# Optimization experiments

Hardware: AMD Instinct MI355X
Metric: run time of the kernel (lower is better)

The kernel has to match this reference:

```python
import jax, jax.numpy as jnp
import numpy as np

B, D, H, W = 16, 512, 32, 32   # batch, input_dim, spatial
CD, K = 256, 8192              # codebook dim, num codes
COMMIT = 1.0


def setup_inputs() -> dict:
    key = jax.random.key(0)
    k0, k1, k2, k3 = jax.random.split(key, 4)
    x = jax.random.normal(k0, (B, D, H, W), dtype=jnp.float32)
    # project_in: Linear(D -> CD); project_out: Linear(CD -> D)
    W_in = jax.random.normal(k1, (CD, D), dtype=jnp.float32) * (1.0 / np.sqrt(D))
    b_in = jnp.zeros((CD,), dtype=jnp.float32)
    W_out = jax.random.normal(k2, (D, CD), dtype=jnp.float32) * (1.0 / np.sqrt(CD))
    b_out = jnp.zeros((D,), dtype=jnp.float32)
    codebook = jax.random.normal(k3, (K, CD), dtype=jnp.float32) * 0.05
    return {"x": x, "W_in": W_in, "b_in": b_in, "W_out": W_out,
            "b_out": b_out, "codebook": codebook}


def reference(x, W_in, b_in, W_out, b_out, codebook):
    b, d, h, w = x.shape
    # b d h w -> b (h w) d
    xt = x.reshape(b, d, h * w).transpose(0, 2, 1)
    z = xt @ W_in.T + b_in                              # [b, n, CD]
    # squared euclidean distances to all codes: ||z||^2 - 2 z.e + ||e||^2
    d2 = ((z * z).sum(-1, keepdims=True)
          - 2.0 * jnp.einsum('bnc,kc->bnk', z, codebook)
          + (codebook * codebook).sum(-1))              # [b, n, K]
    indices = jnp.argmin(d2, axis=-1)                   # [b, n] int
    q = codebook[indices]                               # [b, n, CD]
    # training branch: commitment loss + straight-through estimator
    commitment_loss = COMMIT * jnp.mean((jax.lax.stop_gradient(q) - z) ** 2)
    q_ste = z + jax.lax.stop_gradient(q - z)
    out = q_ste @ W_out.T + b_out                       # [b, n, d]
    out = out.transpose(0, 2, 1).reshape(b, d, h, w)    # b (h w) d -> b d h w
    return out, indices, commitment_loss
```

## Files before the change

### kernel.cpp

```cpp
#include <hip/hip_runtime.h>
#include <cfloat>
#include <cstdint>

#define B_      16
#define DIN     512
#define HW      1024
#define CDIM    256
#define KCODES  8192
#define NTOK    (B_ * HW)
#define OUT_ELEMS (B_ * DIN * HW)
#define NSTRIP  8
#define NPART2  64
#define CPS     (KCODES / NSTRIP)
#define MAXR    4096
#define RCHUNK  32
#define RBLOCKS 2048
#define LOSS_SCALE (1.0f / ((float)NTOK * (float)CDIM))
#define WSCALE      16.0f
#define INV_WS      0.0625f
#define INV_WS2     0.00390625f
#define NEG2_INV_WS (-0.125f)
#define BAND_SLACK  2e-3f

typedef __attribute__((ext_vector_type(8))) _Float16 f16x8;
typedef __attribute__((ext_vector_type(4))) float f32x4;

static __device__ __forceinline__ short f2h(float f) {
  _Float16 h = (_Float16)f;
  return __builtin_bit_cast(short, h);
}
static __device__ __forceinline__ float h2f(short h) {
  return (float)__builtin_bit_cast(_Float16, h);
}

#define GLL16(gsrc, ldst)                                                      \
  __builtin_amdgcn_global_load_lds(                                           \
      (const __attribute__((address_space(1))) unsigned int*)(gsrc),          \
      (__attribute__((address_space(3))) unsigned int*)(ldst), 16, 0, 0)

#define PREP_CB_BLKS 2048
#define PREP_W_BLKS  128
#define PREP_X_BLKS  2048
__global__ __launch_bounds__(256) void k_prep(
    const float* __restrict__ cb, const float* __restrict__ Win,
    const float* __restrict__ Wout, const float* __restrict__ x,
    short* __restrict__ cb_hi, short* __restrict__ cb_lo, float* __restrict__ ee,
    short* __restrict__ wi_hi, short* __restrict__ wi_lo,
    short* __restrict__ wo_hi,
    short* __restrict__ xT_hi, short* __restrict__ xT_lo,
    float* __restrict__ loss, int* __restrict__ rcount, int* __restrict__ scal) {
  __shared__ float T[64][65];
  const int blk = blockIdx.x;
  const int tid = threadIdx.x;
  if (blk == 0 && tid < 2) {
    if (tid == 0) *loss = 0.0f; else *rcount = 0;
  }
  if (blk < PREP_CB_BLKS) {
    const int wid = (blk * 256 + tid) >> 6;
    const int lane = tid & 63;
    const float4 v = *(const float4*)(cb + (size_t)wid * CDIM + lane * 4);
    float s = v.x * v.x + v.y * v.y + v.z * v.z + v.w * v.w;
    const float sx = v.x * WSCALE, sy = v.y * WSCALE,
                sz = v.z * WSCALE, sw = v.w * WSCALE;
    short4 h, l;
    h.x = f2h(sx); l.x = f2h(sx - h2f(h.x));
    h.y = f2h(sy); l.y = f2h(sy - h2f(h.y));
    h.z = f2h(sz); l.z = f2h(sz - h2f(h.z));
    h.w = f2h(sw); l.w = f2h(sw - h2f(h.w));
    *(short4*)(cb_hi + (size_t)wid * CDIM + lane * 4) = h;
    *(short4*)(cb_lo + (size_t)wid * CDIM + lane * 4) = l;
    const float rx = v.x - h2f(h.x) * INV_WS;
    const float ry = v.y - h2f(h.y) * INV_WS;
    const float rz = v.z - h2f(h.z) * INV_WS;
    const float rw = v.w - h2f(h.w) * INV_WS;
    float rr = rx * rx + ry * ry + rz * rz + rw * rw;
#pragma unroll
    for (int off = 32; off > 0; off >>= 1) {
      s += __shfl_down(s, off, 64);
      rr += __shfl_down(rr, off, 64);
    }
    const int wv = tid >> 6;
    if (lane == 0) { ee[wid] = s; T[0][wv] = s; T[1][wv] = rr; }
    __syncthreads();
    if (tid == 0) {
      const float em = fmaxf(fmaxf(T[0][0], T[0][1]), fmaxf(T[0][2], T[0][3]));
      const float rm = fmaxf(fmaxf(T[1][0], T[1][1]), fmaxf(T[1][2], T[1][3]));
      atomicMax(scal + 0, __float_as_int(em));
      atomicMax(scal + 1, __float_as_int(rm));
    }
  } else if (blk < PREP_CB_BLKS + PREP_W_BLKS) {
    const int i = ((blk - PREP_CB_BLKS) * 256 + tid) * 4;
    {
      const float4 v = *(const float4*)(Win + i);
      const float sx = v.x * WSCALE, sy = v.y * WSCALE,
                  sz = v.z * WSCALE, sw = v.w * WSCALE;
      short4 h, l;
      h.x = f2h(sx); l.x = f2h(sx - h2f(h.x));
      h.y = f2h(sy); l.y = f2h(sy - h2f(h.y));
      h.z = f2h(sz); l.z = f2h(sz - h2f(h.z));
      h.w = f2h(sw); l.w = f2h(sw - h2f(h.w));
      *(short4*)(wi_hi + i) = h; *(short4*)(wi_lo + i) = l;
    }
    {
      const float4 v = *(const float4*)(Wout + i);
      short4 h;
      h.x = f2h(v.x * WSCALE);
      h.y = f2h(v.y * WSCALE);
      h.z = f2h(v.z * WSCALE);
      h.w = f2h(v.w * WSCALE);
      *(short4*)(wo_hi + i) = h;
    }
  } else {
    const int id = blk - PREP_CB_BLKS - PREP_W_BLKS;
    const int xb = id & 255, yb = id >> 8;
    const int b = xb >> 4;
    const int hw0 = (xb & 15) * 64;
    const int din0 = yb * 64;
    {
      const int r = tid >> 2;
      const int c = tid & 3;
      const float* src = x + ((size_t)b * DIN + din0 + r) * HW + hw0 + c * 16;
#pragma unroll
      for (int j = 0; j < 4; ++j) {
        const float4 v = *(const float4*)(src + j * 4);
        T[r][c * 16 + j * 4 + 0] = v.x;
        T[r][c * 16 + j * 4 + 1] = v.y;
        T[r][c * 16 + j * 4 + 2] = v.z;
        T[r][c * 16 + j * 4 + 3] = v.w;
      }
    }
    __syncthreads();
    {
      const int tt = tid & 63;
      const int c2 = tid >> 6;
      short h[16], l[16];
#pragma unroll
      for (int j = 0; j < 16; ++j) {
        const float f = T[c2 * 16 + j][tt];
        h[j] = f2h(f); l[j] = f2h(f - h2f(h[j]));
      }
      const size_t base = ((size_t)b * HW + hw0 + tt) * DIN + din0 + c2 * 16;
      *(f16x8*)(xT_hi + base)     = *(f16x8*)&h[0];
      *(f16x8*)(xT_hi + base + 8) = *(f16x8*)&h[8];
      *(f16x8*)(xT_lo + base)     = *(f16x8*)&l[0];
      *(f16x8*)(xT_lo + base + 8) = *(f16x8*)&l[8];
    }
  }
}

__global__ __launch_bounds__(256, 2) void k_proj_in_mfma(
    const short* __restrict__ xT_hi, const short* __restrict__ xT_lo,
    const short* __restrict__ wi_hi, const short* __restrict__ wi_lo,
    const float* __restrict__ bin,
    short* __restrict__ z_hi, short* __restrict__ z_lo) {
  __shared__ short lds_s[4 * 128 * 32];
  char* ldsc = (char*)lds_s;
  const int tid = threadIdx.x;
  const int w = tid >> 6, lane = tid & 63;
  const int quad = lane >> 4, l16 = lane & 15;
  const int wm = w >> 1, wn = w & 1;
  const int tok0 = blockIdx.x * 128;
  const int cd0 = blockIdx.y * 128;

  const int uA = (w << 6) + lane, uB = uA + 256;
  const int tA = uA >> 2, pA = uA & 3, qA = pA ^ ((tA >> 1) & 3);
  const int tB = uB >> 2, pB = uB & 3, qB = pB ^ ((tB >> 1) & 3);
  const int offA = tA * DIN + qA * 8;
  const int offB = tB * DIN + qB * 8;
  const short* gAh0 = xT_hi + (size_t)tok0 * DIN + offA;
  const short* gAh1 = xT_hi + (size_t)tok0 * DIN + offB;
  const short* gAl0 = xT_lo + (size_t)tok0 * DIN + offA;
  const short* gAl1 = xT_lo + (size_t)tok0 * DIN + offB;
  const short* gBh0 = wi_hi + (size_t)cd0 * DIN + offA;
  const short* gBh1 = wi_hi + (size_t)cd0 * DIN + offB;
  const short* gBl0 = wi_lo + (size_t)cd0 * DIN + offA;
  const short* gBl1 = wi_lo + (size_t)cd0 * DIN + offB;

  int aoffs[4], boffs[4];
#pragma unroll
  for (int mi = 0; mi < 4; ++mi) {
    const int t = wm * 64 + mi * 16 + l16;
    aoffs[mi] = t * 64 + (quad ^ ((t >> 1) & 3)) * 16;
  }
#pragma unroll
  for (int ni = 0; ni < 4; ++ni) {
    const int t = wn * 64 + ni * 16 + l16;
    boffs[ni] = 16384 + t * 64 + (quad ^ ((t >> 1) & 3)) * 16;
  }

  f32x4 acc[4][4];
#pragma unroll
  for (int mi = 0; mi < 4; ++mi)
#pragma unroll
    for (int ni = 0; ni < 4; ++ni) acc[mi][ni] = (f32x4){0.f, 0.f, 0.f, 0.f};

  for (int kb = 0; kb < DIN; kb += 32) {
    __syncthreads();
    GLL16(gAh0 + kb, ldsc + ((0 * 4 + w) << 10));
    GLL16(gAh1 + kb, ldsc + ((1 * 4 + w) << 10));
    GLL16(gAl0 + kb, ldsc + ((2 * 4 + w) << 10));
    GLL16(gAl1 + kb, ldsc + ((3 * 4 + w) << 10));
    GLL16(gBh0 + kb, ldsc + ((4 * 4 + w) << 10));
    GLL16(gBh1 + kb, ldsc + ((5 * 4 + w) << 10));
    GLL16(gBl0 + kb, ldsc + ((6 * 4 + w) << 10));
    GLL16(gBl1 + kb, ldsc + ((7 * 4 + w) << 10));
    __syncthreads();
    f16x8 ah[4], al[4], bh[4], bl[4];
#pragma unroll
    for (int mi = 0; mi < 4; ++mi) {
      ah[mi] = *(const f16x8*)(ldsc + aoffs[mi]);
      al[mi] = *(const f16x8*)(ldsc + 8192 + aoffs[mi]);
    }
#pragma unroll
    for (int ni = 0; ni < 4; ++ni) {
      bh[ni] = *(const f16x8*)(ldsc + boffs[ni]);
      bl[ni] = *(const f16x8*)(ldsc + 8192 + boffs[ni]);
    }
#pragma unroll
    for (int mi = 0; mi < 4; ++mi)
#pragma unroll
      for (int ni = 0; ni < 4; ++ni) {
        f32x4 c = acc[mi][ni];
        c = __builtin_amdgcn_mfma_f32_16x16x32_f16(ah[mi], bh[ni], c, 0, 0, 0);
        c = __builtin_amdgcn_mfma_f32_16x16x32_f16(ah[mi], bl[ni], c, 0, 0, 0);
        c = __builtin_amdgcn_mfma_f32_16x16x32_f16(al[mi], bh[ni], c, 0, 0, 0);
        acc[mi][ni] = c;
      }
  }
  float bv[4];
#pragma unroll
  for (int ni = 0; ni < 4; ++ni) bv[ni] = bin[cd0 + wn * 64 + ni * 16 + l16];
#pragma unroll
  for (int mi = 0; mi < 4; ++mi)
#pragma unroll
    for (int r = 0; r < 4; ++r) {
      const int t = tok0 + wm * 64 + mi * 16 + quad * 4 + r;
#pragma unroll
      for (int ni = 0; ni < 4; ++ni) {
        const int cd = cd0 + wn * 64 + ni * 16 + l16;
        const float o = acc[mi][ni][r] * INV_WS + bv[ni];
        const short h = f2h(o);
        z_hi[(size_t)t * CDIM + cd] = h;
        z_lo[(size_t)t * CDIM + cd] = f2h(o - h2f(h));
      }
    }
}

__global__ __launch_bounds__(256, 2) void k_argmin_mfma(
    const short* __restrict__ z_hi,
    const short* __restrict__ cb_hi,
    const float* __restrict__ ee,
    float* __restrict__ pm1v, int* __restrict__ pm1i, float* __restrict__ pm2v) {
  __shared__ short lds_s[2 * 128 * 32];
  char* ldsc = (char*)lds_s;
  const int tid = threadIdx.x;
  const int w = tid >> 6, lane = tid & 63;
  const int quad = lane >> 4, l16 = lane & 15;
  const int wm = w >> 1, wn = w & 1;
  const int tok0 = blockIdx.x * 128;
  const int cbase = blockIdx.y * CPS;

  const int uA = (w << 6) + lane, uB = uA + 256;
  const int tA = uA >> 2, pA = uA & 3, qA = pA ^ ((tA >> 1) & 3);
  const int tB = uB >> 2, pB = uB & 3, qB = pB ^ ((tB >> 1) & 3);
  const int offA = tA * CDIM + qA * 8;
  const int offB = tB * CDIM + qB * 8;
  const short* gAh0 = z_hi + (size_t)tok0 * CDIM + offA;
  const short* gAh1 = z_hi + (size_t)tok0 * CDIM + offB;

  int aoffs[4], boffs[4];
#pragma unroll
  for (int mi = 0; mi < 4; ++mi) {
    const int t = wm * 64 + mi * 16 + l16;
    aoffs[mi] = t * 64 + (quad ^ ((t >> 1) & 3)) * 16;
  }
#pragma unroll
  for (int ni = 0; ni < 4; ++ni) {
    const int t = wn * 64 + ni * 16 + l16;
    boffs[ni] = 8192 + t * 64 + (quad ^ ((t >> 1) & 3)) * 16;
  }

  float mv[16], sv[16]; int mi_[16];
#pragma unroll
  for (int j = 0; j < 16; ++j) {
    mv[j] = FLT_MAX; sv[j] = FLT_MAX; mi_[j] = 0x7fffffff;
  }

  for (int ct = 0; ct < CPS / 128; ++ct) {
    const int ctile = cbase + ct * 128;
    const short* gBh0 = cb_hi + (size_t)ctile * CDIM + offA;
    const short* gBh1 = cb_hi + (size_t)ctile * CDIM + offB;
    f32x4 acc[4][4];
#pragma unroll
    for (int mi = 0; mi < 4; ++mi)
#pragma unroll
      for (int ni = 0; ni < 4; ++ni) acc[mi][ni] = (f32x4){0.f, 0.f, 0.f, 0.f};

    for (int kb = 0; kb < CDIM; kb += 32) {
      __syncthreads();
      GLL16(gAh0 + kb, ldsc + ((0 * 4 + w) << 10));
      GLL16(gAh1 + kb, ldsc + ((1 * 4 + w) << 10));
      GLL16(gBh0 + kb, ldsc + ((2 * 4 + w) << 10));
      GLL16(gBh1 + kb, ldsc + ((3 * 4 + w) << 10));
      __syncthreads();
      f16x8 ah[4], bh[4];
#pragma unroll
      for (int mi = 0; mi < 4; ++mi)
        ah[mi] = *(const f16x8*)(ldsc + aoffs[mi]);
#pragma unroll
      for (int ni = 0; ni < 4; ++ni)
        bh[ni] = *(const f16x8*)(ldsc + boffs[ni]);
#pragma unroll
      for (int mi = 0; mi < 4; ++mi)
#pragma unroll
        for (int ni = 0; ni < 4; ++ni)
          acc[mi][ni] = __builtin_amdgcn_mfma_f32_16x16x32_f16(
              ah[mi], bh[ni], acc[mi][ni], 0, 0, 0);
    }
    float eev[4];
#pragma unroll
    for (int ni = 0; ni < 4; ++ni) eev[ni] = ee[ctile + wn * 64 + ni * 16 + l16];
    const int cb2 = ctile + wn * 64 + l16;
#pragma unroll
    for (int mi = 0; mi < 4; ++mi)
#pragma unroll
      for (int r = 0; r < 4; ++r) {
        const int j = mi * 4 + r;
#pragma unroll
        for (int ni = 0; ni < 4; ++ni) {
          const float s = fmaf(NEG2_INV_WS, acc[mi][ni][r], eev[ni]);
          sv[j] = fminf(sv[j], fmaxf(mv[j], s));
          if (s < mv[j]) { mv[j] = s; mi_[j] = cb2 + ni * 16; }
        }
      }
  }
#pragma unroll
  for (int off = 1; off <= 2; off <<= 1) {
#pragma unroll
    for (int j = 0; j < 16; ++j) {
      const float ov = __shfl_xor(mv[j], off, 64);
      const int   oi = __shfl_xor(mi_[j], off, 64);
      const float os = __shfl_xor(sv[j], off, 64);
      const float snew = fminf(fminf(sv[j], os), fmaxf(mv[j], ov));
      if (ov < mv[j] || (ov == mv[j] && oi < mi_[j])) { mv[j] = ov; mi_[j] = oi; }
      sv[j] = snew;
    }
  }
  if ((l16 & 3) == 0) {
    const int pp = (blockIdx.y * 2 + wn) * 4 + (l16 >> 2);
#pragma unroll
    for (int j = 0; j < 16; ++j) {
      const int mi = j >> 2, r = j & 3;
      const int t = tok0 + wm * 64 + mi * 16 + quad * 4 + r;
      const size_t o = (size_t)t * NPART2 + pp;
      pm1v[o] = mv[j]; pm1i[o] = mi_[j]; pm2v[o] = sv[j];
    }
  }
}

__global__ __launch_bounds__(256) void k_merge_rescue(
    const float* __restrict__ pm1v, const int* __restrict__ pm1i,
    const float* __restrict__ pm2v,
    const short* __restrict__ z_hi, const short* __restrict__ z_lo,
    const float* __restrict__ cb, const int* __restrict__ scal,
    int* __restrict__ idxi, float* __restrict__ idx_f,
    int* __restrict__ rlist, int* __restrict__ rcount,
    float* __restrict__ loss) {
  __shared__ float lpart[4];
  const int tid = threadIdx.x;
  const int wv = tid >> 6, lane = tid & 63;
  const int t = blockIdx.x * 4 + wv;
  const size_t po = (size_t)t * NPART2 + lane;
  const float av = pm1v[po];
  const int   ai = pm1i[po];
  const float asv = pm2v[po];
  float m1v = av; int m1i = ai; float msv = asv;
#pragma unroll
  for (int off = 1; off < 64; off <<= 1) {
    const float ov = __shfl_xor(m1v, off, 64);
    const int   oi = __shfl_xor(m1i, off, 64);
    const float os = __shfl_xor(msv, off, 64);
    msv = fminf(msv, os);
    if (ov < m1v || (ov == m1v && oi < m1i)) { m1v = ov; m1i = oi; }
  }
  const short4 h4 = *(const short4*)(z_hi + (size_t)t * CDIM + lane * 4);
  const short4 l4 = *(const short4*)(z_lo + (size_t)t * CDIM + lane * 4);
  const float hx = h2f(h4.x), hy = h2f(h4.y), hz = h2f(h4.z), hw = h2f(h4.w);
  const float lx = h2f(l4.x), ly = h2f(l4.y), lz = h2f(l4.z), lw = h2f(l4.w);
  const float zx = hx + lx, zy = hy + ly, zz = hz + lz, zw = hw + lw;
  float zl2 = lx * lx + ly * ly + lz * lz + lw * lw;
  float zh2 = hx * hx + hy * hy + hz * hz + hw * hw;
#pragma unroll
  for (int off = 32; off > 0; off >>= 1) {
    zl2 += __shfl_xor(zl2, off, 64);
    zh2 += __shfl_xor(zh2, off, 64);
  }
  const float emax = sqrtf(__int_as_float(scal[0]));
  const float rmax = sqrtf(__int_as_float(scal[1]));
  const float band = 4.0f * (sqrtf(zl2) * emax + sqrtf(zh2) * rmax) + BAND_SLACK;
  const float thr = m1v + band;
  const unsigned long long ball = __ballot(av <= thr);
  const bool flag = (msv <= thr);
  int besti = m1i;
  if (__popcll(ball) > 1) {
    double bestv = 1e300; int bi = 0x7fffffff;
    unsigned long long bb = ball;
    while (bb) {
      const int c = __ffsll((long long)bb) - 1;
      bb &= bb - 1;
      const int ci = __shfl(ai, c, 64);
      const float4 ev = *(const float4*)(cb + (size_t)ci * CDIM + lane * 4);
      const double dx = (double)zx - (double)ev.x;
      const double dy = (double)zy - (double)ev.y;
      const double dz_ = (double)zz - (double)ev.z;
      const double dw = (double)zw - (double)ev.w;
      double d = dx * dx + dy * dy + dz_ * dz_ + dw * dw;
#pragma unroll
      for (int off = 32; off > 0; off >>= 1) d += __shfl_xor(d, off, 64);
      if (d < bestv || (d == bestv && ci < bi)) { bestv = d; bi = ci; }
    }
    besti = bi;
  }
  const float4 qv = *(const float4*)(cb + (size_t)besti * CDIM + lane * 4);
  const float dx = qv.x - zx;
  const float dy = qv.y - zy;
  const float dz_ = qv.z - zz;
  const float dw = qv.w - zw;
  float s = dx * dx + dy * dy + dz_ * dz_ + dw * dw;
#pragma unroll
  for (int off = 32; off > 0; off >>= 1) s += __shfl_down(s, off, 64);
  if (lane == 0) {
    idxi[t] = besti;
    idx_f[t] = (float)besti;
    lpart[wv] = s;
    if (flag) {
      const int pos = atomicAdd(rcount, 1);
      if (pos < MAXR) rlist[pos] = t;
    }
  }
  __syncthreads();
  if (tid == 0) {
    atomicAdd(loss, (lpart[0] + lpart[1] + lpart[2] + lpart[3]) * LOSS_SCALE);
  }
}

__global__ __launch_bounds__(256) void k_rescue_chunk(
    const short* __restrict__ z_hi, const short* __restrict__ z_lo,
    const float* __restrict__ cb,
    const int* __restrict__ rlist, const int* __restrict__ rcount,
    double* __restrict__ slotv, int* __restrict__ sloti) {
  const int cnt0 = *rcount;
  const int cnt = cnt0 < MAXR ? cnt0 : MAXR;
  const int li0 = blockIdx.x >> 5;
  const int chunk = blockIdx.x & (RCHUNK - 1);
  if (li0 >= cnt) return;
  __shared__ float zrow[CDIM];
  __shared__ double rv[256];
  __shared__ int ri[256];
  const int tid = threadIdx.x;
  for (int li = li0; li < cnt; li += RBLOCKS / RCHUNK) {
    const int t = rlist[li];
    zrow[tid] = h2f(z_hi[(size_t)t * CDIM + tid]) + h2f(z_lo[(size_t)t * CDIM + tid]);
    __syncthreads();
    const int k = chunk * 256 + tid;
    const float* e = cb + (size_t)k * CDIM;
    double s0 = 0.0, s1 = 0.0, s2 = 0.0, s3 = 0.0;
    for (int c = 0; c < CDIM; c += 4) {
      const float4 ev = *(const float4*)(e + c);
      const double d0 = (double)zrow[c]     - (double)ev.x;
      const double d1 = (double)zrow[c + 1] - (double)ev.y;
      const double d2 = (double)zrow[c + 2] - (double)ev.z;
      const double d3 = (double)zrow[c + 3] - (double)ev.w;
      s0 += d0 * d0; s1 += d1 * d1; s2 += d2 * d2; s3 += d3 * d3;
    }
    rv[tid] = (s0 + s1) + (s2 + s3);
    ri[tid] = k;
    __syncthreads();
    for (int off = 128; off > 0; off >>= 1) {
      if (tid < off) {
        if (rv[tid + off] < rv[tid] ||
            (rv[tid + off] == rv[tid] && ri[tid + off] < ri[tid])) {
          rv[tid] = rv[tid + off]; ri[tid] = ri[tid + off];
        }
      }
      __syncthreads();
    }
    if (tid == 0) {
      slotv[(size_t)li * RCHUNK + chunk] = rv[0];
      sloti[(size_t)li * RCHUNK + chunk] = ri[0];
    }
    __syncthreads();
  }
}

__global__ __launch_bounds__(256) void k_rescue_fin(
    const double* __restrict__ slotv, const int* __restrict__ sloti,
    const int* __restrict__ rlist, const int* __restrict__ rcount,
    const short* __restrict__ z_hi, const short* __restrict__ z_lo,
    const float* __restrict__ cb,
    int* __restrict__ idxi, float* __restrict__ idx_f, float* __restrict__ loss) {
  const int cnt0 = *rcount;
  const int cnt = cnt0 < MAXR ? cnt0 : MAXR;
  const int tid = threadIdx.x;
  const int wv = tid >> 6, lane = tid & 63;
  for (int li = wv; li < cnt; li += 4) {
    double bv = 1e300; int bx = 0x7fffffff;
    if (lane < RCHUNK) {
      bv = slotv[(size_t)li * RCHUNK + lane];
      bx = sloti[(size_t)li * RCHUNK + lane];
    }
#pragma unroll
    for (int off = 1; off < 32; off <<= 1) {
      const double ov = __shfl_xor(bv, off, 64);
      const int   oi = __shfl_xor(bx, off, 64);
      if (ov < bv || (ov == bv && oi < bx)) { bv = ov; bx = oi; }
    }
    const int newi = __shfl(bx, 0, 64);
    const int t = rlist[li];
    const int oldi = idxi[t];
    if (newi != oldi) {
      const short4 h4 = *(const short4*)(z_hi + (size_t)t * CDIM + lane * 4);
      const short4 l4 = *(const short4*)(z_lo + (size_t)t * CDIM + lane * 4);
      const float4 qn = *(const float4*)(cb + (size_t)newi * CDIM + lane * 4);
      const float4 qo = *(const float4*)(cb + (size_t)oldi * CDIM + lane * 4);
      const float zx = h2f(h4.x) + h2f(l4.x);
      const float zy = h2f(h4.y) + h2f(l4.y);
      const float zz = h2f(h4.z) + h2f(l4.z);
      const float zw = h2f(h4.w) + h2f(l4.w);
      float d = (qn.x - zx) * (qn.x - zx) - (qo.x - zx) * (qo.x - zx)
              + (qn.y - zy) * (qn.y - zy) - (qo.y - zy) * (qo.y - zy)
              + (qn.z - zz) * (qn.z - zz) - (qo.z - zz) * (qo.z - zz)
              + (qn.w - zw) * (qn.w - zw) - (qo.w - zw) * (qo.w - zw);
#pragma unroll
      for (int off = 32; off > 0; off >>= 1) d += __shfl_down(d, off, 64);
      if (lane == 0) {
        idxi[t] = newi;
        idx_f[t] = (float)newi;
        atomicAdd(loss, d * LOSS_SCALE);
      }
    }
  }
}

__global__ __launch_bounds__(256, 2) void k_proj_out_mfma(
    const short* __restrict__ wo_hi,
    const short* __restrict__ cb_hi, const short* __restrict__ cb_lo,
    const int* __restrict__ idxi, const float* __restrict__ bout,
    float* __restrict__ out) {
  __shared__ short lds_s[3 * 128 * 32];
  char* ldsc = (char*)lds_s;
  const int tid = threadIdx.x;
  const int w = tid >> 6, lane = tid & 63;
  const int quad = lane >> 4, l16 = lane & 15;
  const int wm = w >> 1, wn = w & 1;
  const int tok0 = blockIdx.x * 128;
  const int din0 = blockIdx.y * 128;

  const int uA = (w << 6) + lane, uB = uA + 256;
  const int tA = uA >> 2, pA = uA & 3, qA = pA ^ ((tA >> 1) & 3);
  const int tB = uB >> 2, pB = uB & 3, qB = pB ^ ((tB >> 1) & 3);
  const short* gAh0 = wo_hi + (size_t)(din0 + tA) * CDIM + qA * 8;
  const short* gAh1 = wo_hi + (size_t)(din0 + tB) * CDIM + qB * 8;
  const int iA = idxi[tok0 + tA];
  const int iB = idxi[tok0 + tB];
  const short* gBh0 = cb_hi + (size_t)iA * CDIM + qA * 8;
  const short* gBh1 = cb_hi + (size_t)iB * CDIM + qB * 8;
  const short* gBl0 = cb_lo + (size_t)iA * CDIM + qA * 8;
  const short* gBl1 = cb_lo + (size_t)iB * CDIM + qB * 8;

  int aoffs[4], boffs[4];
#pragma unroll
  for (int mi = 0; mi < 4; ++mi) {
    const int t = wm * 64 + mi * 16 + l16;
    aoffs[mi] = t * 64 + (quad ^ ((t >> 1) & 3)) * 16;
  }
#pragma unroll
  for (int ni = 0; ni < 4; ++ni) {
    const int t = wn * 64 + ni * 16 + l16;
    boffs[ni] = 8192 + t * 64 + (quad ^ ((t >> 1) & 3)) * 16;
  }

  f32x4 acc[4][4];
#pragma unroll
  for (int mi = 0; mi < 4; ++mi)
#pragma unroll
    for (int ni = 0; ni < 4; ++ni) acc[mi][ni] = (f32x4){0.f, 0.f, 0.f, 0.f};

  for (int kb = 0; kb < CDIM; kb += 32) {
    __syncthreads();
    GLL16(gAh0 + kb, ldsc + ((0 * 4 + w) << 10));
    GLL16(gAh1 + kb, ldsc + ((1 * 4 + w) << 10));
    GLL16(gBh0 + kb, ldsc + ((2 * 4 + w) << 10));
    GLL16(gBh1 + kb, ldsc + ((3 * 4 + w) << 10));
    GLL16(gBl0 + kb, ldsc + ((4 * 4 + w) << 10));
    GLL16(gBl1 + kb, ldsc + ((5 * 4 + w) << 10));
    __syncthreads();
    f16x8 ah[4], bh[4], bl[4];
#pragma unroll
    for (int mi = 0; mi < 4; ++mi)
      ah[mi] = *(const f16x8*)(ldsc + aoffs[mi]);
#pragma unroll
    for (int ni = 0; ni < 4; ++ni) {
      bh[ni] = *(const f16x8*)(ldsc + boffs[ni]);
      bl[ni] = *(const f16x8*)(ldsc + 8192 + boffs[ni]);
    }
#pragma unroll
    for (int mi = 0; mi < 4; ++mi)
#pragma unroll
      for (int ni = 0; ni < 4; ++ni) {
        f32x4 c = acc[mi][ni];
        c = __builtin_amdgcn_mfma_f32_16x16x32_f16(ah[mi], bh[ni], c, 0, 0, 0);
        c = __builtin_amdgcn_mfma_f32_16x16x32_f16(ah[mi], bl[ni], c, 0, 0, 0);
        acc[mi][ni] = c;
      }
  }
  const int b = tok0 >> 10;
  const int hwb = tok0 & (HW - 1);
  float* ob = out + (size_t)b * DIN * HW;
#pragma unroll
  for (int mi = 0; mi < 4; ++mi)
#pragma unroll
    for (int r = 0; r < 4; ++r) {
      const int din = din0 + wm * 64 + mi * 16 + quad * 4 + r;
      const float bb = bout[din];
#pragma unroll
      for (int ni = 0; ni < 4; ++ni) {
        const int hw = hwb + wn * 64 + ni * 16 + l16;
        ob[(size_t)din * HW + hw] = acc[mi][ni][r] * INV_WS2 + bb;
      }
    }
}

extern "C" void kernel_launch(void* const* d_in, const int* in_sizes, int n_in,
                              void* d_out, int out_size, void* d_ws, size_t ws_size,
                              hipStream_t stream) {
  const float* x    = (const float*)d_in[0];
  const float* Win  = (const float*)d_in[1];
  const float* bin  = (const float*)d_in[2];
  const float* Wout = (const float*)d_in[3];
  const float* bout = (const float*)d_in[4];
  const float* cb   = (const float*)d_in[5];

  float* out   = (float*)d_out;
  float* idx_f = out + OUT_ELEMS;
  float* loss  = out + OUT_ELEMS + NTOK;

  char* w = (char*)d_ws;
  size_t off = 0;
  short* z_hi  = (short*)(w + off); off += (size_t)NTOK * CDIM * 2;
  short* z_lo  = (short*)(w + off); off += (size_t)NTOK * CDIM * 2;
  short* cb_hi = (short*)(w + off); off += (size_t)KCODES * CDIM * 2;
  short* cb_lo = (short*)(w + off); off += (size_t)KCODES * CDIM * 2;
  short* xT_hi = (short*)(w + off); off += (size_t)NTOK * DIN * 2;
  short* xT_lo = (short*)(w + off); off += (size_t)NTOK * DIN * 2;
  short* wi_hi = (short*)(w + off); off += (size_t)CDIM * DIN * 2;
  short* wi_lo = (short*)(w + off); off += (size_t)CDIM * DIN * 2;
  short* wo_hi = (short*)(w + off); off += (size_t)DIN * CDIM * 2;
  float* ee    = (float*)(w + off); off += (size_t)KCODES * 4;
  int*   idxi  = (int*)(w + off);   off += (size_t)NTOK * 4;
  float* pm1v  = (float*)(w + off); off += (size_t)NPART2 * NTOK * 4;
  int*   pm1i  = (int*)(w + off);   off += (size_t)NPART2 * NTOK * 4;
  float* pm2v  = (float*)(w + off); off += (size_t)NPART2 * NTOK * 4;
  int*   rlist = (int*)(w + off);   off += (size_t)MAXR * 4;
  int*   rcount= (int*)(w + off);   off += 256;
  int*   scal  = (int*)(w + off);   off += 256;
  double* slotv= (double*)(w + off);off += (size_t)MAXR * RCHUNK * 8;
  int*   sloti = (int*)(w + off);   off += (size_t)MAXR * RCHUNK * 4;

  hipMemsetAsync(scal, 0, 8, stream);
  k_prep        <<<dim3(PREP_CB_BLKS + PREP_W_BLKS + PREP_X_BLKS),
                   dim3(256), 0, stream>>>(cb, Win, Wout, x, cb_hi, cb_lo, ee,
                                           wi_hi, wi_lo, wo_hi,
                                           xT_hi, xT_lo, loss, rcount, scal);
  k_proj_in_mfma<<<dim3(NTOK / 128, CDIM / 128), dim3(256), 0, stream>>>(
      xT_hi, xT_lo, wi_hi, wi_lo, bin, z_hi, z_lo);
  k_argmin_mfma <<<dim3(NTOK / 128, NSTRIP), dim3(256), 0, stream>>>(
      z_hi, cb_hi, ee, pm1v, pm1i, pm2v);
  k_merge_rescue<<<dim3(NTOK / 4), dim3(256), 0, stream>>>(
      pm1v, pm1i, pm2v, z_hi, z_lo, cb, scal, idxi, idx_f,
      rlist, rcount, loss);
  k_rescue_chunk<<<dim3(RBLOCKS), dim3(256), 0, stream>>>(
      z_hi, z_lo, cb, rlist, rcount, slotv, sloti);
  k_rescue_fin  <<<dim3(1), dim3(256), 0, stream>>>(
      slotv, sloti, rlist, rcount, z_hi, z_lo, cb, idxi, idx_f, loss);
  k_proj_out_mfma<<<dim3(NTOK / 128, DIN / 128), dim3(256), 0, stream>>>(
      wo_hi, cb_hi, cb_lo, idxi, bout, out);
}
```

Measured before the change: 399.6 us.

## Keep token tile resident in LDS and double-buffer codebook loads in argmin

The argmin kernel now loads the whole 128x256 fp16 token tile into LDS once, instead of reloading it for every codebook tile. Codebook chunks are double-buffered so the next chunk's global-to-LDS load is issued before the current MFMAs, and each k-step needs one barrier instead of two. The partial-min output layout changes to [strip][token][8] so the strip stores are contiguous, and the merge kernel's indexing is updated to match. LDS use rises from 16KB to about 80KB per block, which may stop two blocks from sharing a CU under the launch bounds of 2.

```diff
diff --git a/kernel.cpp b/kernel.cpp
--- a/kernel.cpp
+++ b/kernel.cpp
@@ -251,7 +251,7 @@
     const short* __restrict__ cb_hi,
     const float* __restrict__ ee,
     float* __restrict__ pm1v, int* __restrict__ pm1i, float* __restrict__ pm2v) {
-  __shared__ short lds_s[2 * 128 * 32];
+  __shared__ short lds_s[(8 + 2) * 128 * 32];
   char* ldsc = (char*)lds_s;
   const int tid = threadIdx.x;
   const int w = tid >> 6, lane = tid & 63;
@@ -267,6 +267,7 @@
   const int offB = tB * CDIM + qB * 8;
   const short* gAh0 = z_hi + (size_t)tok0 * CDIM + offA;
   const short* gAh1 = z_hi + (size_t)tok0 * CDIM + offB;
+  const short* cbB = cb_hi + (size_t)cbase * CDIM;
 
   int aoffs[4], boffs[4];
 #pragma unroll
@@ -277,7 +278,7 @@
 #pragma unroll
   for (int ni = 0; ni < 4; ++ni) {
     const int t = wn * 64 + ni * 16 + l16;
-    boffs[ni] = 8192 + t * 64 + (quad ^ ((t >> 1) & 3)) * 16;
+    boffs[ni] = t * 64 + (quad ^ ((t >> 1) & 3)) * 16;
   }
 
   float mv[16], sv[16]; int mi_[16];
@@ -286,37 +287,51 @@
     mv[j] = FLT_MAX; sv[j] = FLT_MAX; mi_[j] = 0x7fffffff;
   }
 
-  for (int ct = 0; ct < CPS / 128; ++ct) {
-    const int ctile = cbase + ct * 128;
-    const short* gBh0 = cb_hi + (size_t)ctile * CDIM + offA;
-    const short* gBh1 = cb_hi + (size_t)ctile * CDIM + offB;
+#pragma unroll
+  for (int c = 0; c < 8; ++c) {
+    GLL16(gAh0 + c * 32, ldsc + c * 8192 + (w << 10));
+    GLL16(gAh1 + c * 32, ldsc + c * 8192 + 4096 + (w << 10));
+  }
+  GLL16(cbB + offA, ldsc + 65536 + (w << 10));
+  GLL16(cbB + offB, ldsc + 65536 + 4096 + (w << 10));
+  __syncthreads();
+
+  int buf = 0;
+  for (int ct = 0; ct < 8; ++ct) {
     f32x4 acc[4][4];
 #pragma unroll
     for (int mi = 0; mi < 4; ++mi)
 #pragma unroll
       for (int ni = 0; ni < 4; ++ni) acc[mi][ni] = (f32x4){0.f, 0.f, 0.f, 0.f};
 
-    for (int kb = 0; kb < CDIM; kb += 32) {
-      __syncthreads();
-      GLL16(gAh0 + kb, ldsc + ((0 * 4 + w) << 10));
-      GLL16(gAh1 + kb, ldsc + ((1 * 4 + w) << 10));
-      GLL16(gBh0 + kb, ldsc + ((2 * 4 + w) << 10));
-      GLL16(gBh1 + kb, ldsc + ((3 * 4 + w) << 10));
-      __syncthreads();
+    for (int kbi = 0; kbi < 8; ++kbi) {
+      const int step = ct * 8 + kbi;
+      if (step + 1 < 64) {
+        const int ns = step + 1;
+        const size_t nbase = ((size_t)(ns >> 3) << 15) + ((ns & 7) << 5);
+        char* bdst = ldsc + 65536 + ((buf ^ 1) << 13);
+        GLL16(cbB + nbase + offA, bdst + (w << 10));
+        GLL16(cbB + nbase + offB, bdst + 4096 + (w << 10));
+      }
+      const int abase = kbi << 13;
+      const char* bbase = ldsc + 65536 + (buf << 13);
       f16x8 ah[4], bh[4];
 #pragma unroll
       for (int mi = 0; mi < 4; ++mi)
-        ah[mi] = *(const f16x8*)(ldsc + aoffs[mi]);
+        ah[mi] = *(const f16x8*)(ldsc + abase + aoffs[mi]);
 #pragma unroll
       for (int ni = 0; ni < 4; ++ni)
-        bh[ni] = *(const f16x8*)(ldsc + boffs[ni]);
+        bh[ni] = *(const f16x8*)(bbase + boffs[ni]);
 #pragma unroll
       for (int mi = 0; mi < 4; ++mi)
 #pragma unroll
         for (int ni = 0; ni < 4; ++ni)
           acc[mi][ni] = __builtin_amdgcn_mfma_f32_16x16x32_f16(
               ah[mi], bh[ni], acc[mi][ni], 0, 0, 0);
-    }
+      __syncthreads();
+      buf ^= 1;
+    }
+    const int ctile = cbase + ct * 128;
     float eev[4];
 #pragma unroll
     for (int ni = 0; ni < 4; ++ni) eev[ni] = ee[ctile + wn * 64 + ni * 16 + l16];
@@ -347,12 +362,12 @@
     }
   }
   if ((l16 & 3) == 0) {
-    const int pp = (blockIdx.y * 2 + wn) * 4 + (l16 >> 2);
+    const int sub = wn * 4 + (l16 >> 2);
 #pragma unroll
     for (int j = 0; j < 16; ++j) {
       const int mi = j >> 2, r = j & 3;
       const int t = tok0 + wm * 64 + mi * 16 + quad * 4 + r;
-      const size_t o = (size_t)t * NPART2 + pp;
+      const size_t o = ((size_t)blockIdx.y * NTOK + t) * 8 + sub;
       pm1v[o] = mv[j]; pm1i[o] = mi_[j]; pm2v[o] = sv[j];
     }
   }
@@ -370,7 +385,7 @@
   const int tid = threadIdx.x;
   const int wv = tid >> 6, lane = tid & 63;
   const int t = blockIdx.x * 4 + wv;
-  const size_t po = (size_t)t * NPART2 + lane;
+  const size_t po = ((size_t)(lane >> 3) * NTOK + t) * 8 + (lane & 7);
   const float av = pm1v[po];
   const int   ai = pm1i[po];
   const float asv = pm2v[po];
```

Result: faster. 387.7 us (-3.0%).

## Keep token tile resident in LDS and stream codebook directly into registers

Applied to the files above, without the earlier changes.

The argmin kernel now loads a 64-token by full-depth tile of z into LDS once, with a 512-thread block. Each wave streams its own 64 codes straight from global memory into registers with double buffering, removing the per-k-step barriers and LDS staging of the codebook. Partial minima are reduced across the 16 lanes, and the partial-result layout is transposed to [partition][token], with the merge kernel's indexing updated to match. The trade is more global traffic for codebook fragments that are not shared through LDS, plus different occupancy from the larger block and the 32 KB LDS tile.

```diff
diff --git a/kernel.cpp b/kernel.cpp
--- a/kernel.cpp
+++ b/kernel.cpp
@@ -246,38 +246,33 @@
     }
 }
 
-__global__ __launch_bounds__(256, 2) void k_argmin_mfma(
+__global__ __launch_bounds__(512) void k_argmin_mfma(
     const short* __restrict__ z_hi,
     const short* __restrict__ cb_hi,
     const float* __restrict__ ee,
     float* __restrict__ pm1v, int* __restrict__ pm1i, float* __restrict__ pm2v) {
-  __shared__ short lds_s[2 * 128 * 32];
+  __shared__ short lds_s[64 * 256];
   char* ldsc = (char*)lds_s;
   const int tid = threadIdx.x;
   const int w = tid >> 6, lane = tid & 63;
   const int quad = lane >> 4, l16 = lane & 15;
-  const int wm = w >> 1, wn = w & 1;
-  const int tok0 = blockIdx.x * 128;
+  const int tok0 = blockIdx.x * 64;
   const int cbase = blockIdx.y * CPS;
 
-  const int uA = (w << 6) + lane, uB = uA + 256;
-  const int tA = uA >> 2, pA = uA & 3, qA = pA ^ ((tA >> 1) & 3);
-  const int tB = uB >> 2, pB = uB & 3, qB = pB ^ ((tB >> 1) & 3);
-  const int offA = tA * CDIM + qA * 8;
-  const int offB = tB * CDIM + qB * 8;
-  const short* gAh0 = z_hi + (size_t)tok0 * CDIM + offA;
-  const short* gAh1 = z_hi + (size_t)tok0 * CDIM + offB;
-
-  int aoffs[4], boffs[4];
+#pragma unroll
+  for (int r = 0; r < 4; ++r) {
+    const int u = r * 512 + tid;
+    const int c = u >> 8, tA = (u >> 2) & 63, pA = u & 3;
+    const int qA = pA ^ ((tA >> 1) & 3);
+    GLL16(z_hi + (size_t)(tok0 + tA) * CDIM + c * 32 + qA * 8,
+          ldsc + r * 8192 + (w << 10));
+  }
+
+  int aoffs[4];
 #pragma unroll
   for (int mi = 0; mi < 4; ++mi) {
-    const int t = wm * 64 + mi * 16 + l16;
+    const int t = mi * 16 + l16;
     aoffs[mi] = t * 64 + (quad ^ ((t >> 1) & 3)) * 16;
-  }
-#pragma unroll
-  for (int ni = 0; ni < 4; ++ni) {
-    const int t = wn * 64 + ni * 16 + l16;
-    boffs[ni] = 8192 + t * 64 + (quad ^ ((t >> 1) & 3)) * 16;
   }
 
   float mv[16], sv[16]; int mi_[16];
@@ -286,41 +281,47 @@
     mv[j] = FLT_MAX; sv[j] = FLT_MAX; mi_[j] = 0x7fffffff;
   }
 
-  for (int ct = 0; ct < CPS / 128; ++ct) {
-    const int ctile = cbase + ct * 128;
-    const short* gBh0 = cb_hi + (size_t)ctile * CDIM + offA;
-    const short* gBh1 = cb_hi + (size_t)ctile * CDIM + offB;
+  __syncthreads();
+
+#pragma unroll
+  for (int pass = 0; pass < 2; ++pass) {
+    const int c0 = cbase + pass * 512 + w * 64;
+    const short* bb = cb_hi + (size_t)(c0 + l16) * CDIM + quad * 8;
     f32x4 acc[4][4];
 #pragma unroll
     for (int mi = 0; mi < 4; ++mi)
 #pragma unroll
       for (int ni = 0; ni < 4; ++ni) acc[mi][ni] = (f32x4){0.f, 0.f, 0.f, 0.f};
 
-    for (int kb = 0; kb < CDIM; kb += 32) {
-      __syncthreads();
-      GLL16(gAh0 + kb, ldsc + ((0 * 4 + w) << 10));
-      GLL16(gAh1 + kb, ldsc + ((1 * 4 + w) << 10));
-      GLL16(gBh0 + kb, ldsc + ((2 * 4 + w) << 10));
-      GLL16(gBh1 + kb, ldsc + ((3 * 4 + w) << 10));
-      __syncthreads();
-      f16x8 ah[4], bh[4];
+    f16x8 bA[4], bB[4];
+#pragma unroll
+    for (int ni = 0; ni < 4; ++ni)
+      bA[ni] = *(const f16x8*)(bb + (size_t)ni * 16 * CDIM);
+#pragma unroll
+    for (int s = 0; s < 8; ++s) {
+      if (s < 7) {
+#pragma unroll
+        for (int ni = 0; ni < 4; ++ni) {
+          const f16x8 v =
+              *(const f16x8*)(bb + (size_t)ni * 16 * CDIM + (s + 1) * 32);
+          if (s & 1) bA[ni] = v; else bB[ni] = v;
+        }
+      }
+      f16x8 ah[4];
 #pragma unroll
       for (int mi = 0; mi < 4; ++mi)
-        ah[mi] = *(const f16x8*)(ldsc + aoffs[mi]);
-#pragma unroll
-      for (int ni = 0; ni < 4; ++ni)
-        bh[ni] = *(const f16x8*)(ldsc + boffs[ni]);
+        ah[mi] = *(const f16x8*)(ldsc + (s << 12) + aoffs[mi]);
 #pragma unroll
       for (int mi = 0; mi < 4; ++mi)
 #pragma unroll
         for (int ni = 0; ni < 4; ++ni)
           acc[mi][ni] = __builtin_amdgcn_mfma_f32_16x16x32_f16(
-              ah[mi], bh[ni], acc[mi][ni], 0, 0, 0);
+              ah[mi], (s & 1) ? bB[ni] : bA[ni], acc[mi][ni], 0, 0, 0);
     }
     float eev[4];
 #pragma unroll
-    for (int ni = 0; ni < 4; ++ni) eev[ni] = ee[ctile + wn * 64 + ni * 16 + l16];
-    const int cb2 = ctile + wn * 64 + l16;
+    for (int ni = 0; ni < 4; ++ni) eev[ni] = ee[c0 + ni * 16 + l16];
+    const int cb2 = c0 + l16;
 #pragma unroll
     for (int mi = 0; mi < 4; ++mi)
 #pragma unroll
@@ -335,7 +336,7 @@
       }
   }
 #pragma unroll
-  for (int off = 1; off <= 2; off <<= 1) {
+  for (int off = 1; off < 16; off <<= 1) {
 #pragma unroll
     for (int j = 0; j < 16; ++j) {
       const float ov = __shfl_xor(mv[j], off, 64);
@@ -346,13 +347,13 @@
       sv[j] = snew;
     }
   }
-  if ((l16 & 3) == 0) {
-    const int pp = (blockIdx.y * 2 + wn) * 4 + (l16 >> 2);
+  if (l16 == 0) {
+    const int p = blockIdx.y * 8 + w;
 #pragma unroll
     for (int j = 0; j < 16; ++j) {
       const int mi = j >> 2, r = j & 3;
-      const int t = tok0 + wm * 64 + mi * 16 + quad * 4 + r;
-      const size_t o = (size_t)t * NPART2 + pp;
+      const int t = tok0 + mi * 16 + quad * 4 + r;
+      const size_t o = (size_t)p * NTOK + t;
       pm1v[o] = mv[j]; pm1i[o] = mi_[j]; pm2v[o] = sv[j];
     }
   }
@@ -370,7 +371,7 @@
   const int tid = threadIdx.x;
   const int wv = tid >> 6, lane = tid & 63;
   const int t = blockIdx.x * 4 + wv;
-  const size_t po = (size_t)t * NPART2 + lane;
+  const size_t po = (size_t)lane * NTOK + t;
   const float av = pm1v[po];
   const int   ai = pm1i[po];
   const float asv = pm2v[po];
@@ -674,7 +675,7 @@
                                            xT_hi, xT_lo, loss, rcount, scal);
   k_proj_in_mfma<<<dim3(NTOK / 128, CDIM / 128), dim3(256), 0, stream>>>(
       xT_hi, xT_lo, wi_hi, wi_lo, bin, z_hi, z_lo);
-  k_argmin_mfma <<<dim3(NTOK / 128, NSTRIP), dim3(256), 0, stream>>>(
+  k_argmin_mfma <<<dim3(NTOK / 64, NSTRIP), dim3(512), 0, stream>>>(
       z_hi, cb_hi, ee, pm1v, pm1i, pm2v);
   k_merge_rescue<<<dim3(NTOK / 4), dim3(256), 0, stream>>>(
       pm1v, pm1i, pm2v, z_hi, z_lo, cb, scal, idxi, idx_f,
```

Result: slower. 555.3 us (+39.0%).
